# Kernel tuning notes

Hardware: AMD Instinct MI355X
Metric: run time of the kernel (lower is better)

Reference implementation:

```python
import jax, jax.numpy as jnp
import numpy as np


def _gru(x, W, U, return_sequences):
    """Keras GRU, reset_after=True, recurrent_activation=sigmoid, activation=linear, no bias.
    x: [B,T,D], W: [D,3D] input kernel, U: [D,3D] recurrent kernel."""
    D = U.shape[0]
    xW = jnp.einsum('btd,de->bte', x, W)  # precompute input projections [B,T,3D]

    def step(h, xw_t):
        hu = h @ U  # [B,3D]
        xz, xr, xh = jnp.split(xw_t, 3, axis=-1)
        uz, ur, uh = jnp.split(hu, 3, axis=-1)
        z = jax.nn.sigmoid(xz + uz)          # update gate
        r = jax.nn.sigmoid(xr + ur)          # reset gate
        hh = xh + r * uh                     # candidate, linear activation, reset_after=True
        h_new = z * h + (1.0 - z) * hh
        return h_new, h_new

    h0 = jnp.zeros((x.shape[0], D), dtype=x.dtype)
    hT, hs = jax.lax.scan(step, h0, jnp.swapaxes(xW, 0, 1))  # scan over time
    return jnp.swapaxes(hs, 0, 1) if return_sequences else hT


def setup_inputs() -> dict:
    key = jax.random.key(0)
    ks = jax.random.split(key, 6)
    B, T, D = 16384, 25, 128
    s = 0.05  # keep gate pre-activations in a sane range
    return {
        "x": jax.random.normal(ks[0], (B, T, D), jnp.float32),
        "W1": jax.random.normal(ks[1], (D, 3 * D), jnp.float32) * s,
        "U1": jax.random.normal(ks[2], (D, 3 * D), jnp.float32) * s,
        "W2": jax.random.normal(ks[3], (D, 3 * D), jnp.float32) * s,
        "U2": jax.random.normal(ks[4], (D, 3 * D), jnp.float32) * s,
        "Wout": jax.random.normal(ks[5], (D, D), jnp.float32) * s,
    }


def reference(x, W1, U1, W2, U2, Wout):
    h1 = _gru(x, W1, U1, True)    # [B,T,D]
    h2 = _gru(h1, W2, U2, False)  # [B,D] last state
    return h2 @ Wout              # [B,D]
```

## Files before the change

kernel.cpp:

```cpp
#include <hip/hip_runtime.h>


typedef _Float16 half8 __attribute__((ext_vector_type(8)));
typedef __fp16  fp16x2 __attribute__((ext_vector_type(2)));
typedef float f32x4 __attribute__((ext_vector_type(4)));

#define MFMA(a, b, c) __builtin_amdgcn_mfma_f32_16x16x32_f16((a), (b), (c), 0, 0, 0)

constexpr int T_STEPS = 25;
constexpr int D = 128;
constexpr int NG = 384;
constexpr int BT = 64;
constexpr int SH = 136;
constexpr int SX = 132;

typedef const __attribute__((address_space(1))) unsigned int guint;
typedef __attribute__((address_space(3))) unsigned int luint;

__device__ __forceinline__ void load_lds4(const float* g, float* l) {
    __builtin_amdgcn_global_load_lds((guint*)(uintptr_t)g, (luint*)l, 4, 0, 0);
}

__device__ __forceinline__ float sigm(float v) {
    return __builtin_amdgcn_rcpf(1.0f + __expf(-v));
}

__global__ __launch_bounds__(1024, 4) void gru2_kernel(
    const float* __restrict__ x, const float* __restrict__ W1,
    const float* __restrict__ U1, const float* __restrict__ W2,
    const float* __restrict__ U2, const float* __restrict__ Wout,
    float* __restrict__ out) {
    __shared__ float    X[2][BT * SX];
    __shared__ _Float16 H1[2][BT * SH];
    __shared__ _Float16 H2[2][BT * SH];

    const int tid = threadIdx.x;
    const int w = tid >> 6, lane = tid & 63, l15 = lane & 15, quad = lane >> 4;
    const int layer = w >> 3;
    const int d0 = (w & 7) * 16;
    const int b0 = blockIdx.x * BT;

    half8 wg[3][8];
    {
        const float* Wp = layer ? W2 : W1;
        const float* Up = layer ? U2 : U1;
#pragma unroll
        for (int g = 0; g < 3; ++g) {
            const int c = g * 128 + d0 + l15;
#pragma unroll
            for (int k = 0; k < 8; ++k) {
                const float* src = (k < 4 ? Wp : Up) + (size_t)((k & 3) * 32 + quad * 8) * NG + c;
                half8 f;
#pragma unroll
                for (int e = 0; e < 8; ++e) f[e] = (_Float16)src[(size_t)e * NG];
                wg[g][k] = f;
            }
        }
    }

    for (int idx = tid; idx < BT * SH; idx += 1024) {
        H1[0][idx] = (_Float16)0.f;
        H2[1][idx] = (_Float16)0.f;
    }

#pragma unroll
    for (int r8 = 0; r8 < 8; ++r8) {
        const int idx = w * 8 + r8, row = idx >> 1, hf = (idx & 1) * 64;
        load_lds4(x + ((size_t)(b0 + row) * T_STEPS + 0) * D + hf + lane,
                  &X[0][row * SX + hf]);
    }

    __syncthreads();

#pragma unroll 1
    for (int it = 0; it <= T_STEPS; ++it) {
        const int p = it & 1, q = p ^ 1;
        if (it + 1 < T_STEPS) {
#pragma unroll
            for (int r8 = 0; r8 < 8; ++r8) {
                const int idx = w * 8 + r8, row = idx >> 1, hf = (idx & 1) * 64;
                load_lds4(x + ((size_t)(b0 + row) * T_STEPS + (it + 1)) * D + hf + lane,
                          &X[q][row * SX + hf]);
            }
        }
        const bool active = layer ? (it >= 1) : (it < T_STEPS);
        if (active) {
            const _Float16* Hst = layer ? H2[p] : H1[p];
            _Float16* Hout      = layer ? H2[q] : H1[q];
            const _Float16* Hin = H1[p];
            const float* Xin    = X[p];
#pragma unroll
            for (int m = 0; m < 4; ++m) {
                const int arow = m * 16 + l15;
                f32x4 cz = {0.f, 0.f, 0.f, 0.f}, cr = {0.f, 0.f, 0.f, 0.f};
                f32x4 cxh = {0.f, 0.f, 0.f, 0.f}, cuh = {0.f, 0.f, 0.f, 0.f};
#pragma unroll
                for (int k = 0; k < 4; ++k) {
                    half8 A;
                    if (!layer) {
                        const float* ap = Xin + arow * SX + quad * 8 + k * 32;
                        const float4 v0 = *(const float4*)(ap);
                        const float4 v1 = *(const float4*)(ap + 4);
                        union { fp16x2 h2[4]; half8 h8; } u;
                        u.h2[0] = __builtin_amdgcn_cvt_pkrtz(v0.x, v0.y);
                        u.h2[1] = __builtin_amdgcn_cvt_pkrtz(v0.z, v0.w);
                        u.h2[2] = __builtin_amdgcn_cvt_pkrtz(v1.x, v1.y);
                        u.h2[3] = __builtin_amdgcn_cvt_pkrtz(v1.z, v1.w);
                        A = u.h8;
                    } else {
                        A = *(const half8*)(Hin + arow * SH + quad * 8 + k * 32);
                    }
                    cz  = MFMA(A, wg[0][k], cz);
                    cr  = MFMA(A, wg[1][k], cr);
                    cxh = MFMA(A, wg[2][k], cxh);
                }
#pragma unroll
                for (int k = 0; k < 4; ++k) {
                    const half8 A = *(const half8*)(Hst + arow * SH + quad * 8 + k * 32);
                    cz  = MFMA(A, wg[0][4 + k], cz);
                    cr  = MFMA(A, wg[1][4 + k], cr);
                    cuh = MFMA(A, wg[2][4 + k], cuh);
                }
#pragma unroll
                for (int i2 = 0; i2 < 4; ++i2) {
                    const int row = m * 16 + quad * 4 + i2;
                    const float hp = (float)Hst[row * SH + d0 + l15];
                    const float z = sigm(cz[i2]);
                    const float r = sigm(cr[i2]);
                    const float hh = cxh[i2] + r * cuh[i2];
                    const float hn = hh + z * (hp - hh);
                    Hout[row * SH + d0 + l15] = (_Float16)hn;
                }
            }
        }
        __syncthreads();
    }

    if (layer) {
        const int col = d0 + l15;
        half8 wO[4];
#pragma unroll
        for (int k = 0; k < 4; ++k) {
            half8 f;
#pragma unroll
            for (int e = 0; e < 8; ++e)
                f[e] = (_Float16)Wout[(size_t)(k * 32 + quad * 8 + e) * D + col];
            wO[k] = f;
        }
#pragma unroll
        for (int m = 0; m < 4; ++m) {
            const _Float16* ap = H2[0] + (m * 16 + l15) * SH + quad * 8;
            f32x4 acc = {0.f, 0.f, 0.f, 0.f};
#pragma unroll
            for (int k = 0; k < 4; ++k) {
                const half8 A = *(const half8*)(ap + k * 32);
                acc = MFMA(A, wO[k], acc);
            }
#pragma unroll
            for (int i2 = 0; i2 < 4; ++i2)
                out[(size_t)(b0 + m * 16 + quad * 4 + i2) * D + col] = acc[i2];
        }
    }
}

extern "C" void kernel_launch(void* const* d_in, const int* in_sizes, int n_in,
                              void* d_out, int out_size, void* d_ws, size_t ws_size,
                              hipStream_t stream) {
    const float* x    = (const float*)d_in[0];
    const float* W1   = (const float*)d_in[1];
    const float* U1   = (const float*)d_in[2];
    const float* W2   = (const float*)d_in[3];
    const float* U2   = (const float*)d_in[4];
    const float* Wout = (const float*)d_in[5];
    gru2_kernel<<<dim3(16384 / BT), dim3(1024), 0, stream>>>(
        x, W1, U1, W2, U2, Wout, (float*)d_out);
}
```

Before: 514.4 us.

## Transpose MFMA operands, pre-convert x to fp16 in LDS, pin weights in AGPRs

Swaps the MFMA operand roles so the weights are the A operand and the batch rows are B. Each lane now owns four contiguous hidden units of one batch row, which lets the h-state read/write and the output store be vectorized. The x tile is converted once per step from an fp32 staging buffer into an fp16 padded buffer shared by all waves, removing the redundant per-wave cvt work. The cost is an extra barrier per step, and because there is only one fp32 staging buffer, the prefetch for the next step has to wait until conversion finishes. Weight fragments are also forced into AGPRs via inline asm to relieve VGPR pressure.

```diff
diff --git a/kernel.cpp b/kernel.cpp
--- a/kernel.cpp
+++ b/kernel.cpp
@@ -3,7 +3,8 @@
 
 typedef _Float16 half8 __attribute__((ext_vector_type(8)));
 typedef __fp16  fp16x2 __attribute__((ext_vector_type(2)));
-typedef float f32x4 __attribute__((ext_vector_type(4)));
+typedef __fp16  fp16x4 __attribute__((ext_vector_type(4)));
+typedef float    f32x4 __attribute__((ext_vector_type(4)));
 
 #define MFMA(a, b, c) __builtin_amdgcn_mfma_f32_16x16x32_f16((a), (b), (c), 0, 0, 0)
 
@@ -12,7 +13,6 @@
 constexpr int NG = 384;
 constexpr int BT = 64;
 constexpr int SH = 136;
-constexpr int SX = 132;
 
 typedef const __attribute__((address_space(1))) unsigned int guint;
 typedef __attribute__((address_space(3))) unsigned int luint;
@@ -25,12 +25,15 @@
     return __builtin_amdgcn_rcpf(1.0f + __expf(-v));
 }
 
-__global__ __launch_bounds__(1024, 4) void gru2_kernel(
+__global__ __attribute__((amdgpu_flat_work_group_size(1024, 1024),
+                          amdgpu_waves_per_eu(4, 4)))
+void gru2_kernel(
     const float* __restrict__ x, const float* __restrict__ W1,
     const float* __restrict__ U1, const float* __restrict__ W2,
     const float* __restrict__ U2, const float* __restrict__ Wout,
     float* __restrict__ out) {
-    __shared__ float    X[2][BT * SX];
+    __shared__ float    Xf[BT * D];
+    __shared__ _Float16 Xh[2][BT * SH];
     __shared__ _Float16 H1[2][BT * SH];
     __shared__ _Float16 H2[2][BT * SH];
 
@@ -48,15 +51,20 @@
         for (int g = 0; g < 3; ++g) {
             const int c = g * 128 + d0 + l15;
 #pragma unroll
-            for (int k = 0; k < 8; ++k) {
-                const float* src = (k < 4 ? Wp : Up) + (size_t)((k & 3) * 32 + quad * 8) * NG + c;
+            for (int kt = 0; kt < 8; ++kt) {
+                const float* src = (kt < 4 ? Wp : Up) + (size_t)((kt & 3) * 32 + quad * 8) * NG + c;
                 half8 f;
 #pragma unroll
                 for (int e = 0; e < 8; ++e) f[e] = (_Float16)src[(size_t)e * NG];
-                wg[g][k] = f;
+                wg[g][kt] = f;
             }
         }
     }
+#pragma unroll
+    for (int g = 0; g < 3; ++g)
+#pragma unroll
+        for (int kt = 0; kt < 8; ++kt)
+            asm volatile("" : "+a"(wg[g][kt]));
 
     for (int idx = tid; idx < BT * SH; idx += 1024) {
         H1[0][idx] = (_Float16)0.f;
@@ -67,98 +75,94 @@
     for (int r8 = 0; r8 < 8; ++r8) {
         const int idx = w * 8 + r8, row = idx >> 1, hf = (idx & 1) * 64;
         load_lds4(x + ((size_t)(b0 + row) * T_STEPS + 0) * D + hf + lane,
-                  &X[0][row * SX + hf]);
+                  Xf + idx * 64);
     }
-
     __syncthreads();
 
 #pragma unroll 1
     for (int it = 0; it <= T_STEPS; ++it) {
         const int p = it & 1, q = p ^ 1;
+        if (it < T_STEPS) {
+#pragma unroll
+            for (int c = 0; c < 2; ++c) {
+                const int i0 = c * 4096 + tid * 4;
+                const float4 v = *(const float4*)(Xf + i0);
+                const int row = i0 >> 7, col = i0 & 127;
+                union { fp16x2 h2[2]; fp16x4 h4; } u;
+                u.h2[0] = __builtin_amdgcn_cvt_pkrtz(v.x, v.y);
+                u.h2[1] = __builtin_amdgcn_cvt_pkrtz(v.z, v.w);
+                *(fp16x4*)(&Xh[p][row * SH + col]) = u.h4;
+            }
+        }
+        __syncthreads();
         if (it + 1 < T_STEPS) {
 #pragma unroll
             for (int r8 = 0; r8 < 8; ++r8) {
                 const int idx = w * 8 + r8, row = idx >> 1, hf = (idx & 1) * 64;
                 load_lds4(x + ((size_t)(b0 + row) * T_STEPS + (it + 1)) * D + hf + lane,
-                          &X[q][row * SX + hf]);
+                          Xf + idx * 64);
             }
         }
         const bool active = layer ? (it >= 1) : (it < T_STEPS);
         if (active) {
             const _Float16* Hst = layer ? H2[p] : H1[p];
             _Float16* Hout      = layer ? H2[q] : H1[q];
-            const _Float16* Hin = H1[p];
-            const float* Xin    = X[p];
+            const _Float16* Bin = layer ? H1[p] : Xh[p];
 #pragma unroll
-            for (int m = 0; m < 4; ++m) {
-                const int arow = m * 16 + l15;
+            for (int nt = 0; nt < 4; ++nt) {
+                const int bb = nt * 16 + l15;
+                const _Float16* bi = Bin + bb * SH + quad * 8;
+                const _Float16* bs = Hst + bb * SH + quad * 8;
                 f32x4 cz = {0.f, 0.f, 0.f, 0.f}, cr = {0.f, 0.f, 0.f, 0.f};
                 f32x4 cxh = {0.f, 0.f, 0.f, 0.f}, cuh = {0.f, 0.f, 0.f, 0.f};
 #pragma unroll
-                for (int k = 0; k < 4; ++k) {
-                    half8 A;
-                    if (!layer) {
-                        const float* ap = Xin + arow * SX + quad * 8 + k * 32;
-                        const float4 v0 = *(const float4*)(ap);
-                        const float4 v1 = *(const float4*)(ap + 4);
-                        union { fp16x2 h2[4]; half8 h8; } u;
-                        u.h2[0] = __builtin_amdgcn_cvt_pkrtz(v0.x, v0.y);
-                        u.h2[1] = __builtin_amdgcn_cvt_pkrtz(v0.z, v0.w);
-                        u.h2[2] = __builtin_amdgcn_cvt_pkrtz(v1.x, v1.y);
-                        u.h2[3] = __builtin_amdgcn_cvt_pkrtz(v1.z, v1.w);
-                        A = u.h8;
-                    } else {
-                        A = *(const half8*)(Hin + arow * SH + quad * 8 + k * 32);
-                    }
-                    cz  = MFMA(A, wg[0][k], cz);
-                    cr  = MFMA(A, wg[1][k], cr);
-                    cxh = MFMA(A, wg[2][k], cxh);
+                for (int kt = 0; kt < 4; ++kt) {
+                    const half8 B = *(const half8*)(bi + kt * 32);
+                    cz  = MFMA(wg[0][kt], B, cz);
+                    cr  = MFMA(wg[1][kt], B, cr);
+                    cxh = MFMA(wg[2][kt], B, cxh);
                 }
 #pragma unroll
-                for (int k = 0; k < 4; ++k) {
-                    const half8 A = *(const half8*)(Hst + arow * SH + quad * 8 + k * 32);
-                    cz  = MFMA(A, wg[0][4 + k], cz);
-                    cr  = MFMA(A, wg[1][4 + k], cr);
-                    cuh = MFMA(A, wg[2][4 + k], cuh);
+                for (int kt = 0; kt < 4; ++kt) {
+                    const half8 B = *(const half8*)(bs + kt * 32);
+                    cz  = MFMA(wg[0][4 + kt], B, cz);
+                    cr  = MFMA(wg[1][4 + kt], B, cr);
+                    cuh = MFMA(wg[2][4 + kt], B, cuh);
                 }
+                const int hoff = bb * SH + d0 + quad * 4;
+                const fp16x4 hp4 = *(const fp16x4*)(Hst + hoff);
+                fp16x4 hn4;
 #pragma unroll
                 for (int i2 = 0; i2 < 4; ++i2) {
-                    const int row = m * 16 + quad * 4 + i2;
-                    const float hp = (float)Hst[row * SH + d0 + l15];
                     const float z = sigm(cz[i2]);
                     const float r = sigm(cr[i2]);
                     const float hh = cxh[i2] + r * cuh[i2];
-                    const float hn = hh + z * (hp - hh);
-                    Hout[row * SH + d0 + l15] = (_Float16)hn;
+                    hn4[i2] = (__fp16)(hh + z * ((float)hp4[i2] - hh));
                 }
+                *(fp16x4*)(Hout + hoff) = hn4;
             }
         }
         __syncthreads();
     }
 
     if (layer) {
-        const int col = d0 + l15;
         half8 wO[4];
 #pragma unroll
-        for (int k = 0; k < 4; ++k) {
+        for (int kt = 0; kt < 4; ++kt) {
             half8 f;
 #pragma unroll
             for (int e = 0; e < 8; ++e)
-                f[e] = (_Float16)Wout[(size_t)(k * 32 + quad * 8 + e) * D + col];
-            wO[k] = f;
+                f[e] = (_Float16)Wout[(size_t)(kt * 32 + quad * 8 + e) * D + d0 + l15];
+            wO[kt] = f;
         }
 #pragma unroll
-        for (int m = 0; m < 4; ++m) {
-            const _Float16* ap = H2[0] + (m * 16 + l15) * SH + quad * 8;
+        for (int nt = 0; nt < 4; ++nt) {
+            const _Float16* bp = H2[0] + (nt * 16 + l15) * SH + quad * 8;
             f32x4 acc = {0.f, 0.f, 0.f, 0.f};
 #pragma unroll
-            for (int k = 0; k < 4; ++k) {
-                const half8 A = *(const half8*)(ap + k * 32);
-                acc = MFMA(A, wO[k], acc);
-            }
-#pragma unroll
-            for (int i2 = 0; i2 < 4; ++i2)
-                out[(size_t)(b0 + m * 16 + quad * 4 + i2) * D + col] = acc[i2];
+            for (int kt = 0; kt < 4; ++kt)
+                acc = MFMA(wO[kt], *(const half8*)(bp + kt * 32), acc);
+            *(f32x4*)(out + (size_t)(b0 + nt * 16 + l15) * D + d0 + quad * 4) = acc;
         }
     }
 }
```

Result: slower. 922.3 us (+79.3%).
